# Performance work log

Hardware: AMD Instinct MI355X
Metric: run time of the kernel (lower is better)

The kernel has to match this reference:

```python
import jax, jax.numpy as jnp
import numpy as np

IN = 1    # input feature dim (hardcoded in NN)
H = 10    # LSTM hidden size (hardcoded in NN)
B = 8192  # batch
T = 256   # sequence length


def setup_inputs() -> dict:
    key = jax.random.key(0)
    ks = jax.random.split(key, 12)
    s = 0.1  # init scale for mus (mimics blitz posterior_mu_init spread)
    RHO0 = -3.0  # posterior_rho_init from the module
    return {
        "x": jax.random.normal(ks[0], (B, T, IN), jnp.float32),
        # BayesianLSTM variational parameters (blitz layout: (in, 4*H), (H, 4*H), (4*H,))
        "w_ih_mu": jax.random.normal(ks[1], (IN, 4 * H), jnp.float32) * s,
        "w_ih_rho": jnp.full((IN, 4 * H), RHO0, jnp.float32),
        "w_hh_mu": jax.random.normal(ks[2], (H, 4 * H), jnp.float32) * s,
        "w_hh_rho": jnp.full((H, 4 * H), RHO0, jnp.float32),
        "b_mu": jax.random.normal(ks[3], (4 * H,), jnp.float32) * s,
        "b_rho": jnp.full((4 * H,), RHO0, jnp.float32),
        # reparameterization noise, sampled once per forward call in blitz
        "eps_ih": jax.random.normal(ks[4], (IN, 4 * H), jnp.float32),
        "eps_hh": jax.random.normal(ks[5], (H, 4 * H), jnp.float32),
        "eps_b": jax.random.normal(ks[6], (4 * H,), jnp.float32),
        # deterministic linear head nn.Linear(10, 1)
        "lin_w": jax.random.normal(ks[7], (1, H), jnp.float32) * s,
        "lin_b": jnp.zeros((1,), jnp.float32),
    }


def reference(x, w_ih_mu, w_ih_rho, w_hh_mu, w_hh_rho, b_mu, b_rho,
              eps_ih, eps_hh, eps_b, lin_w, lin_b):
    sp = jax.nn.softplus
    # sample weights: w = mu + log1p(exp(rho)) * eps
    w_ih = w_ih_mu + sp(w_ih_rho) * eps_ih   # (IN, 4H)
    w_hh = w_hh_mu + sp(w_hh_rho) * eps_hh   # (H, 4H)
    b = b_mu + sp(b_rho) * eps_b             # (4H,)

    # precompute input contribution for all timesteps: (B, T, 4H)
    x_proj = jnp.einsum('bti,ig->btg', x, w_ih) + b

    def step(carry, xg):
        h, c = carry                      # (B, H) each
        gates = xg + h @ w_hh             # (B, 4H)
        i = jax.nn.sigmoid(gates[:, :H])
        f = jax.nn.sigmoid(gates[:, H:2 * H])
        g = jnp.tanh(gates[:, 2 * H:3 * H])
        o = jax.nn.sigmoid(gates[:, 3 * H:])
        c = f * c + i * g
        h = o * jnp.tanh(c)
        return (h, c), None

    h0 = jnp.zeros((x.shape[0], H), x.dtype)
    (h_last, _), _ = jax.lax.scan(step, (h0, h0), jnp.swapaxes(x_proj, 0, 1))
    # NN takes hidden_seq[:, -1, :] == final hidden state, then linear head
    return h_last @ lin_w.T + lin_b  # (B, 1)
```

## Files before the change

### kernel.cpp

```cpp
#include <hip/hip_runtime.h>
#include <math.h>

#define T_LEN 256
#define HID 10
#define G4 40

typedef float v2f __attribute__((ext_vector_type(2)));

__device__ __forceinline__ v2f mk2(float a, float b) { v2f r; r.x = a; r.y = b; return r; }

__device__ __forceinline__ float softplus_f(float x) {
    return fmaxf(x, 0.0f) + log1pf(expf(-fabsf(x)));
}

__device__ __forceinline__ float samp(const float* mu, const float* rho,
                                      const float* eps, int i) {
    return mu[i] + softplus_f(rho[i]) * eps[i];
}

__device__ __forceinline__ float fast_sigmoid(float x) {
    return __builtin_amdgcn_rcpf(1.0f + __expf(-x));
}

__device__ __forceinline__ float fast_tanh(float x) {
    float e = __expf(2.0f * x);
    return 1.0f - 2.0f * __builtin_amdgcn_rcpf(e + 1.0f);
}

__global__ __launch_bounds__(256) void bayes_lstm_kernel(
    const float* __restrict__ x,
    const float* __restrict__ w_ih_mu, const float* __restrict__ w_ih_rho,
    const float* __restrict__ w_hh_mu, const float* __restrict__ w_hh_rho,
    const float* __restrict__ b_mu,    const float* __restrict__ b_rho,
    const float* __restrict__ eps_ih,  const float* __restrict__ eps_hh,
    const float* __restrict__ eps_b,
    const float* __restrict__ lin_w,   const float* __restrict__ lin_b,
    float* __restrict__ out)
{
    const int tid   = threadIdx.x;
    const int k     = tid & 15;
    const int group = tid >> 4;
    const int b     = blockIdx.x * 16 + group;

    v2f whh01[HID], whh23[HID];
    v2f wih01 = mk2(0.f, 0.f), wih23 = mk2(0.f, 0.f);
    v2f b01   = mk2(0.f, 0.f), b23   = mk2(0.f, 0.f);
#pragma unroll
    for (int j = 0; j < HID; ++j) { whh01[j] = mk2(0.f, 0.f); whh23[j] = mk2(0.f, 0.f); }

    if (k < HID) {
        const int c0 = 0 * HID + k, c1 = 1 * HID + k, c2 = 2 * HID + k, c3 = 3 * HID + k;
        wih01 = mk2(samp(w_ih_mu, w_ih_rho, eps_ih, c0), samp(w_ih_mu, w_ih_rho, eps_ih, c1));
        wih23 = mk2(samp(w_ih_mu, w_ih_rho, eps_ih, c2), samp(w_ih_mu, w_ih_rho, eps_ih, c3));
        b01   = mk2(samp(b_mu, b_rho, eps_b, c0), samp(b_mu, b_rho, eps_b, c1));
        b23   = mk2(samp(b_mu, b_rho, eps_b, c2), samp(b_mu, b_rho, eps_b, c3));
#pragma unroll
        for (int j = 0; j < HID; ++j) {
            whh01[j] = mk2(samp(w_hh_mu, w_hh_rho, eps_hh, j * G4 + c0),
                           samp(w_hh_mu, w_hh_rho, eps_hh, j * G4 + c1));
            whh23[j] = mk2(samp(w_hh_mu, w_hh_rho, eps_hh, j * G4 + c2),
                           samp(w_hh_mu, w_hh_rho, eps_hh, j * G4 + c3));
        }
    }

    float h_all[HID];
#pragma unroll
    for (int j = 0; j < HID; ++j) h_all[j] = 0.0f;
    float c = 0.0f;

    const float* xrow = x + (size_t)b * T_LEN;
    float xcur = xrow[k];

    for (int to = 0; to < 16; ++to) {
        float xnext = 0.0f;
        if (to < 15) xnext = xrow[(to + 1) * 16 + k];

#pragma unroll
        for (int ti = 0; ti < 16; ++ti) {
            float xt = __shfl(xcur, ti, 16);
            v2f xt2 = mk2(xt, xt);
            v2f acc01 = __builtin_elementwise_fma(xt2, wih01, b01);
            v2f acc23 = __builtin_elementwise_fma(xt2, wih23, b23);
#pragma unroll
            for (int j = 0; j < HID; ++j) {
                v2f hj2 = mk2(h_all[j], h_all[j]);
                acc01 = __builtin_elementwise_fma(hj2, whh01[j], acc01);
                acc23 = __builtin_elementwise_fma(hj2, whh23[j], acc23);
            }
            float ig = fast_sigmoid(acc01.x);
            float fg = fast_sigmoid(acc01.y);
            float gg = fast_tanh(acc23.x);
            float og = fast_sigmoid(acc23.y);
            c = fmaf(fg, c, ig * gg);
            float hk = og * fast_tanh(c);
#pragma unroll
            for (int j = 0; j < HID; ++j) h_all[j] = __shfl(hk, j, 16);
        }
        xcur = xnext;
    }

    if (k == 0) {
        float o = lin_b[0];
#pragma unroll
        for (int j = 0; j < HID; ++j) o = fmaf(h_all[j], lin_w[j], o);
        out[b] = o;
    }
}

extern "C" void kernel_launch(void* const* d_in, const int* in_sizes, int n_in,
                              void* d_out, int out_size, void* d_ws, size_t ws_size,
                              hipStream_t stream) {
    const float* x        = (const float*)d_in[0];
    const float* w_ih_mu  = (const float*)d_in[1];
    const float* w_ih_rho = (const float*)d_in[2];
    const float* w_hh_mu  = (const float*)d_in[3];
    const float* w_hh_rho = (const float*)d_in[4];
    const float* b_mu     = (const float*)d_in[5];
    const float* b_rho    = (const float*)d_in[6];
    const float* eps_ih   = (const float*)d_in[7];
    const float* eps_hh   = (const float*)d_in[8];
    const float* eps_b    = (const float*)d_in[9];
    const float* lin_w    = (const float*)d_in[10];
    const float* lin_b    = (const float*)d_in[11];
    float* out = (float*)d_out;

    const int n_b = in_sizes[0] / T_LEN;
    dim3 grid(n_b / 16), block(256);
    hipLaunchKernelGGL(bayes_lstm_kernel, grid, block, 0, stream,
                       x, w_ih_mu, w_ih_rho, w_hh_mu, w_hh_rho, b_mu, b_rho,
                       eps_ih, eps_hh, eps_b, lin_w, lin_b, out);
}
```

Measured before the change: 169.6 us.

## Interleave two batch rows per lane group and broadcast hidden state via LDS

Each 16-lane group now runs two independent LSTM recurrences side by side, so their dependency chains can hide each other's latency. The per-step broadcast of the hidden state moves from ten lane shuffles to LDS writes followed by float4 reads. The recurrent matmul is split into two accumulator chains, and the activations use exp2 intrinsics. The grid is halved, which leaves fewer waves per CU, and the code relies on in-wave ordering of LDS accesses without a barrier.

```diff
diff --git a/kernel.cpp b/kernel.cpp
--- a/kernel.cpp
+++ b/kernel.cpp
@@ -3,28 +3,69 @@
 
 #define T_LEN 256
 #define HID 10
-#define G4 40
 
 typedef float v2f __attribute__((ext_vector_type(2)));
 
 __device__ __forceinline__ v2f mk2(float a, float b) { v2f r; r.x = a; r.y = b; return r; }
+__device__ __forceinline__ v2f splat2(float a) { return mk2(a, a); }
 
 __device__ __forceinline__ float softplus_f(float x) {
     return fmaxf(x, 0.0f) + log1pf(expf(-fabsf(x)));
 }
-
 __device__ __forceinline__ float samp(const float* mu, const float* rho,
                                       const float* eps, int i) {
     return mu[i] + softplus_f(rho[i]) * eps[i];
 }
 
 __device__ __forceinline__ float fast_sigmoid(float x) {
-    return __builtin_amdgcn_rcpf(1.0f + __expf(-x));
+    float e = __builtin_amdgcn_exp2f(-1.442695040888963f * x);
+    return __builtin_amdgcn_rcpf(1.0f + e);
+}
+__device__ __forceinline__ float fast_tanh(float x) {
+    float e = __builtin_amdgcn_exp2f(2.885390081777927f * x);
+    return fmaf(-2.0f, __builtin_amdgcn_rcpf(e + 1.0f), 1.0f);
 }
 
-__device__ __forceinline__ float fast_tanh(float x) {
-    float e = __expf(2.0f * x);
-    return 1.0f - 2.0f * __builtin_amdgcn_rcpf(e + 1.0f);
+struct Wreg {
+    v2f whh01[HID], whh23[HID];
+    v2f wih01, wih23, b01, b23;
+};
+
+__device__ __forceinline__ float lstm_step(const Wreg& w, float xt,
+                                           float4 h0, float4 h1, float4 h2,
+                                           float& c)
+{
+    v2f x2 = splat2(xt);
+    v2f e01 = __builtin_elementwise_fma(x2, w.wih01, w.b01);
+    v2f e23 = __builtin_elementwise_fma(x2, w.wih23, w.b23);
+    v2f o01 = w.whh01[1] * splat2(h0.y);
+    v2f o23 = w.whh23[1] * splat2(h0.y);
+    e01 = __builtin_elementwise_fma(splat2(h0.x), w.whh01[0], e01);
+    e23 = __builtin_elementwise_fma(splat2(h0.x), w.whh23[0], e23);
+    o01 = __builtin_elementwise_fma(splat2(h0.w), w.whh01[3], o01);
+    o23 = __builtin_elementwise_fma(splat2(h0.w), w.whh23[3], o23);
+    e01 = __builtin_elementwise_fma(splat2(h0.z), w.whh01[2], e01);
+    e23 = __builtin_elementwise_fma(splat2(h0.z), w.whh23[2], e23);
+    o01 = __builtin_elementwise_fma(splat2(h1.y), w.whh01[5], o01);
+    o23 = __builtin_elementwise_fma(splat2(h1.y), w.whh23[5], o23);
+    e01 = __builtin_elementwise_fma(splat2(h1.x), w.whh01[4], e01);
+    e23 = __builtin_elementwise_fma(splat2(h1.x), w.whh23[4], e23);
+    o01 = __builtin_elementwise_fma(splat2(h1.w), w.whh01[7], o01);
+    o23 = __builtin_elementwise_fma(splat2(h1.w), w.whh23[7], o23);
+    e01 = __builtin_elementwise_fma(splat2(h1.z), w.whh01[6], e01);
+    e23 = __builtin_elementwise_fma(splat2(h1.z), w.whh23[6], e23);
+    o01 = __builtin_elementwise_fma(splat2(h2.y), w.whh01[9], o01);
+    o23 = __builtin_elementwise_fma(splat2(h2.y), w.whh23[9], o23);
+    e01 = __builtin_elementwise_fma(splat2(h2.x), w.whh01[8], e01);
+    e23 = __builtin_elementwise_fma(splat2(h2.x), w.whh23[8], e23);
+    v2f a01 = e01 + o01;
+    v2f a23 = e23 + o23;
+    float ig = fast_sigmoid(a01.x);
+    float fg = fast_sigmoid(a01.y);
+    float gg = fast_tanh(a23.x);
+    float og = fast_sigmoid(a23.y);
+    c = fmaf(fg, c, ig * gg);
+    return og * fast_tanh(c);
 }
 
 __global__ __launch_bounds__(256) void bayes_lstm_kernel(
@@ -37,73 +78,79 @@
     const float* __restrict__ lin_w,   const float* __restrict__ lin_b,
     float* __restrict__ out)
 {
+    __shared__ __align__(16) float hbuf[16 * 2 * 12];
+
     const int tid   = threadIdx.x;
     const int k     = tid & 15;
-    const int group = tid >> 4;
-    const int b     = blockIdx.x * 16 + group;
+    const int slot  = tid >> 4;
+    const int gslot = blockIdx.x * 16 + slot;
+    const int bA    = gslot * 2, bB = bA + 1;
+    const int ibA   = slot * 24, ibB = ibA + 12;
 
-    v2f whh01[HID], whh23[HID];
-    v2f wih01 = mk2(0.f, 0.f), wih23 = mk2(0.f, 0.f);
-    v2f b01   = mk2(0.f, 0.f), b23   = mk2(0.f, 0.f);
+    Wreg w;
 #pragma unroll
-    for (int j = 0; j < HID; ++j) { whh01[j] = mk2(0.f, 0.f); whh23[j] = mk2(0.f, 0.f); }
-
+    for (int j = 0; j < HID; ++j) { w.whh01[j] = splat2(0.f); w.whh23[j] = splat2(0.f); }
+    w.wih01 = splat2(0.f); w.wih23 = splat2(0.f);
+    w.b01 = splat2(0.f);   w.b23 = splat2(0.f);
+    float lw = 0.f;
     if (k < HID) {
-        const int c0 = 0 * HID + k, c1 = 1 * HID + k, c2 = 2 * HID + k, c3 = 3 * HID + k;
-        wih01 = mk2(samp(w_ih_mu, w_ih_rho, eps_ih, c0), samp(w_ih_mu, w_ih_rho, eps_ih, c1));
-        wih23 = mk2(samp(w_ih_mu, w_ih_rho, eps_ih, c2), samp(w_ih_mu, w_ih_rho, eps_ih, c3));
-        b01   = mk2(samp(b_mu, b_rho, eps_b, c0), samp(b_mu, b_rho, eps_b, c1));
-        b23   = mk2(samp(b_mu, b_rho, eps_b, c2), samp(b_mu, b_rho, eps_b, c3));
+        const int c0 = k, c1 = HID + k, c2 = 2 * HID + k, c3 = 3 * HID + k;
+        w.wih01 = mk2(samp(w_ih_mu, w_ih_rho, eps_ih, c0), samp(w_ih_mu, w_ih_rho, eps_ih, c1));
+        w.wih23 = mk2(samp(w_ih_mu, w_ih_rho, eps_ih, c2), samp(w_ih_mu, w_ih_rho, eps_ih, c3));
+        w.b01   = mk2(samp(b_mu, b_rho, eps_b, c0), samp(b_mu, b_rho, eps_b, c1));
+        w.b23   = mk2(samp(b_mu, b_rho, eps_b, c2), samp(b_mu, b_rho, eps_b, c3));
 #pragma unroll
         for (int j = 0; j < HID; ++j) {
-            whh01[j] = mk2(samp(w_hh_mu, w_hh_rho, eps_hh, j * G4 + c0),
-                           samp(w_hh_mu, w_hh_rho, eps_hh, j * G4 + c1));
-            whh23[j] = mk2(samp(w_hh_mu, w_hh_rho, eps_hh, j * G4 + c2),
-                           samp(w_hh_mu, w_hh_rho, eps_hh, j * G4 + c3));
+            w.whh01[j] = mk2(samp(w_hh_mu, w_hh_rho, eps_hh, j * 4 * HID + c0),
+                             samp(w_hh_mu, w_hh_rho, eps_hh, j * 4 * HID + c1));
+            w.whh23[j] = mk2(samp(w_hh_mu, w_hh_rho, eps_hh, j * 4 * HID + c2),
+                             samp(w_hh_mu, w_hh_rho, eps_hh, j * 4 * HID + c3));
         }
+        lw = lin_w[k];
+        hbuf[ibA + k] = 0.f;
+        hbuf[ibB + k] = 0.f;
     }
 
-    float h_all[HID];
-#pragma unroll
-    for (int j = 0; j < HID; ++j) h_all[j] = 0.0f;
-    float c = 0.0f;
-
-    const float* xrow = x + (size_t)b * T_LEN;
-    float xcur = xrow[k];
+    float cA = 0.f, cB = 0.f, hkA = 0.f, hkB = 0.f;
+    const float* xrA = x + (size_t)bA * T_LEN;
+    const float* xrB = x + (size_t)bB * T_LEN;
+    float xcA = xrA[k];
+    float xcB = xrB[k];
+    const float4* pA = (const float4*)(hbuf + ibA);
+    const float4* pB = (const float4*)(hbuf + ibB);
 
     for (int to = 0; to < 16; ++to) {
-        float xnext = 0.0f;
-        if (to < 15) xnext = xrow[(to + 1) * 16 + k];
-
+        float xnA = 0.f, xnB = 0.f;
+        if (to < 15) {
+            xnA = xrA[(to + 1) * 16 + k];
+            xnB = xrB[(to + 1) * 16 + k];
+        }
 #pragma unroll
         for (int ti = 0; ti < 16; ++ti) {
-            float xt = __shfl(xcur, ti, 16);
-            v2f xt2 = mk2(xt, xt);
-            v2f acc01 = __builtin_elementwise_fma(xt2, wih01, b01);
-            v2f acc23 = __builtin_elementwise_fma(xt2, wih23, b23);
-#pragma unroll
-            for (int j = 0; j < HID; ++j) {
-                v2f hj2 = mk2(h_all[j], h_all[j]);
-                acc01 = __builtin_elementwise_fma(hj2, whh01[j], acc01);
-                acc23 = __builtin_elementwise_fma(hj2, whh23[j], acc23);
+            float4 hA0 = pA[0], hA1 = pA[1], hA2 = pA[2];
+            float4 hB0 = pB[0], hB1 = pB[1], hB2 = pB[2];
+            float xa = __shfl(xcA, ti, 16);
+            float xb = __shfl(xcB, ti, 16);
+            hkA = lstm_step(w, xa, hA0, hA1, hA2, cA);
+            hkB = lstm_step(w, xb, hB0, hB1, hB2, cB);
+            if (k < HID) {
+                hbuf[ibA + k] = hkA;
+                hbuf[ibB + k] = hkB;
             }
-            float ig = fast_sigmoid(acc01.x);
-            float fg = fast_sigmoid(acc01.y);
-            float gg = fast_tanh(acc23.x);
-            float og = fast_sigmoid(acc23.y);
-            c = fmaf(fg, c, ig * gg);
-            float hk = og * fast_tanh(c);
-#pragma unroll
-            for (int j = 0; j < HID; ++j) h_all[j] = __shfl(hk, j, 16);
         }
-        xcur = xnext;
+        xcA = xnA; xcB = xnB;
     }
 
+    float pa = hkA * lw;
+    float pb = hkB * lw;
+    pa += __shfl_xor(pa, 1, 16);  pb += __shfl_xor(pb, 1, 16);
+    pa += __shfl_xor(pa, 2, 16);  pb += __shfl_xor(pb, 2, 16);
+    pa += __shfl_xor(pa, 4, 16);  pb += __shfl_xor(pb, 4, 16);
+    pa += __shfl_xor(pa, 8, 16);  pb += __shfl_xor(pb, 8, 16);
     if (k == 0) {
-        float o = lin_b[0];
-#pragma unroll
-        for (int j = 0; j < HID; ++j) o = fmaf(h_all[j], lin_w[j], o);
-        out[b] = o;
+        float b0 = lin_b[0];
+        out[bA] = pa + b0;
+        out[bB] = pb + b0;
     }
 }
 
@@ -125,7 +172,7 @@
     float* out = (float*)d_out;
 
     const int n_b = in_sizes[0] / T_LEN;
-    dim3 grid(n_b / 16), block(256);
+    dim3 grid(n_b / 32), block(256);
     hipLaunchKernelGGL(bayes_lstm_kernel, grid, block, 0, stream,
                        x, w_ih_mu, w_ih_rho, w_hh_mu, w_hh_rho, b_mu, b_rho,
                        eps_ih, eps_hh, eps_b, lin_w, lin_b, out);
```

Result: faster. 163.9 us (-3.4%).
